# Kernel tuning notes

Hardware: AMD Instinct MI355X
Metric: run time of the kernel (lower is better)

## Reference

```python
import jax, jax.numpy as jnp
import numpy as np

B, S, D = 4, 4096, 1024
GROUP = 256
HEAD = 128
INNER = 2048


def setup_inputs() -> dict:
    key = jax.random.key(0)
    ks = jax.random.split(key, 16)
    s = 0.02
    return {
        'x': jax.random.normal(ks[0], (B, S, D), jnp.float32),
        'Wv': jax.random.normal(ks[1], (D, INNER), jnp.float32) * s,
        'bv': jnp.zeros((INNER,), jnp.float32),
        'Wg': jax.random.normal(ks[2], (D, INNER), jnp.float32) * s,
        'bg': jnp.zeros((INNER,), jnp.float32),
        'Win': jax.random.normal(ks[3], (D, HEAD), jnp.float32) * s,
        'bin_': jnp.zeros((HEAD,), jnp.float32),
        'Wout': jax.random.normal(ks[4], (INNER, D), jnp.float32) * s,
        'bout': jnp.zeros((D,), jnp.float32),
        'g_qq': 1.0 + jax.random.normal(ks[5], (HEAD,), jnp.float32) * s,
        'b_qq': jnp.zeros((HEAD,), jnp.float32),
        'g_qk': 1.0 + jax.random.normal(ks[6], (HEAD,), jnp.float32) * s,
        'b_qk': jnp.zeros((HEAD,), jnp.float32),
        'g_lq': 1.0 + jax.random.normal(ks[7], (HEAD,), jnp.float32) * s,
        'b_lq': jnp.zeros((HEAD,), jnp.float32),
        'g_lk': 1.0 + jax.random.normal(ks[8], (HEAD,), jnp.float32) * s,
        'b_lk': jnp.zeros((HEAD,), jnp.float32),
    }


def reference(x, Wv, bv, Wg, bg, Win, bin_, Wout, bout,
              g_qq, b_qq, g_qk, b_qk, g_lq, b_lq, g_lk, b_lk):
    b, s, d = x.shape
    g = s // GROUP
    xc = x.reshape(b, g, GROUP, d)                       # [B,G,C,D]
    v = jax.nn.silu(xc @ Wv + bv)                        # [B,G,C,E]
    gate = jax.nn.silu(xc @ Wg + bg)                     # [B,G,C,E]
    x_ = jax.nn.silu(xc @ Win + bin_)                    # [B,G,C,H]
    quad_q = x_ * g_qq + b_qq
    quad_k = x_ * g_qk + b_qk
    lin_q = x_ * g_lq + b_lq
    lin_k = x_ * g_lk + b_lk
    # local quadratic relu^2 attention per chunk
    scale = jnp.asarray(INNER ** 0.5, x.dtype)           # v.size(-1)**0.5
    attn = jnp.einsum('bgns,bgms->bgnm', quad_q, quad_k) / scale
    causal_mask = jnp.triu(jnp.ones((GROUP, GROUP), bool), 1)
    attn = jnp.where(causal_mask, 0.0, attn)
    attn = jnp.square(jax.nn.relu(attn))
    v_quad = jnp.einsum('bgnm,bgme->bgne', attn, v)
    # global causal linear attention: exclusive cumsum of per-chunk k^T v over chunks
    kv = jnp.einsum('bgcs,bgce->bgse', lin_k, v)         # [B,G,H,E]
    kv = jnp.cumsum(kv, axis=1) - kv                     # exclusive over chunk dim
    v_lin = jnp.einsum('bgcs,bgse->bgce', lin_q, kv)
    o = (v_quad + v_lin) * gate
    o = o @ Wout + bout
    return o.reshape(b, s, d)
```

## Files before the change

### kernel.cpp

```cpp
#include <hip/hip_runtime.h>

typedef __attribute__((ext_vector_type(8))) short short8;
typedef __attribute__((ext_vector_type(4))) float floatx4;
typedef __attribute__((ext_vector_type(4))) unsigned short ushort4v;
typedef unsigned short u16;

#define DEV __device__ __forceinline__

DEV u16 f2bf(float f) {
  unsigned int u = __float_as_uint(f);
  u += 0x7fffu + ((u >> 16) & 1u);
  return (u16)(u >> 16);
}
DEV float bf2f(u16 h) { return __uint_as_float(((unsigned int)h) << 16); }
DEV float silu_f(float x) { return x / (1.f + __expf(-x)); }
DEV floatx4 fzero() { floatx4 z = {0.f, 0.f, 0.f, 0.f}; return z; }
DEV floatx4 mfma16(short8 a, short8 b, floatx4 c) {
  return __builtin_amdgcn_mfma_f32_16x16x32_bf16(a, b, c, 0, 0, 0);
}
DEV void gll16(const void* g, void* l) {
  __builtin_amdgcn_global_load_lds((__attribute__((address_space(1))) void*)g,
                                   (__attribute__((address_space(3))) void*)l,
                                   16, 0, 0);
}

__global__ __launch_bounds__(256) void cast_x_kernel(const float* __restrict__ x,
                                                     u16* __restrict__ xb, int n4) {
  int i = blockIdx.x * 256 + threadIdx.x;
  if (i >= n4) return;
  float4 v = ((const float4*)x)[i];
  ushort4v o;
  o[0] = f2bf(v.x); o[1] = f2bf(v.y); o[2] = f2bf(v.z); o[3] = f2bf(v.w);
  *(ushort4v*)&xb[(size_t)i * 4] = o;
}

__global__ __launch_bounds__(256) void transpose_cast_kernel(const float* __restrict__ W,
                                                             u16* __restrict__ WT,
                                                             int K, int N) {
  __shared__ u16 tile[32][36];
  int n0 = blockIdx.x * 32, k0 = blockIdx.y * 32;
  int t = threadIdx.x;
  int r = t >> 3, cs = (t & 7) * 4;
  float4 v = *(const float4*)&W[(size_t)(k0 + r) * N + n0 + cs];
  tile[r][cs + 0] = f2bf(v.x);
  tile[r][cs + 1] = f2bf(v.y);
  tile[r][cs + 2] = f2bf(v.z);
  tile[r][cs + 3] = f2bf(v.w);
  __syncthreads();
  ushort4v o;
  o[0] = tile[cs + 0][r];
  o[1] = tile[cs + 1][r];
  o[2] = tile[cs + 2][r];
  o[3] = tile[cs + 3][r];
  *(ushort4v*)&WT[(size_t)(n0 + r) * K + k0 + cs] = o;
}

DEV void wave_transposed_store(u16* __restrict__ Ct, long chunk_stride,
                               const u16* trw, int chunk, int cbase, int nbase,
                               int lane) {
#pragma unroll
  for (int it = 0; it < 8; ++it) {
    int e_l = it * 8 + (lane >> 3);
    int c_off = (lane & 7) * 8;
    short8 val = *(const short8*)&trw[e_l * 72 + c_off];
    *(short8*)&Ct[(size_t)chunk * chunk_stride + (size_t)(nbase + e_l) * 256 + cbase +
                  c_off] = val;
  }
}

__global__ __launch_bounds__(256, 2) void gemm_vg(
    const u16* __restrict__ A, const u16* __restrict__ Bv, const u16* __restrict__ Bg,
    const float* __restrict__ bvb, const float* __restrict__ bgb,
    u16* __restrict__ vT, u16* __restrict__ gate) {
  constexpr int K = 1024, N = 2048;
  __shared__ union {
    struct { u16 a[128 * 64]; u16 b[2][128 * 64]; } st;
    u16 tr[4 * 64 * 72];
  } sm;
  const int t = threadIdx.x;
  const int wave = t >> 6, lane = t & 63;
  const int l15 = lane & 15, l16 = lane >> 4;
  const int ell = blockIdx.x;
  const int xcd = ell & 7, i = ell >> 3;
  const int m0 = (xcd * 16 + (i >> 4)) * 128;
  const int n0 = (i & 15) * 128;
  const int wm = (wave >> 1) * 64, wn = (wave & 1) * 64;

  floatx4 accv[4][4], accg[4][4];
#pragma unroll
  for (int a = 0; a < 4; ++a)
#pragma unroll
    for (int b = 0; b < 4; ++b) { accv[a][b] = fzero(); accg[a][b] = fzero(); }

  const u16 *pa[4], *pbv[4], *pbg[4];
#pragma unroll
  for (int j = 0; j < 4; ++j) {
    const int c = t + 256 * j;
    const int r = c >> 3, p = c & 7;
    const int g = p ^ (r & 7);
    const size_t off = (size_t)r * K + g * 8;
    pa[j] = A + (size_t)m0 * K + off;
    pbv[j] = Bv + (size_t)n0 * K + off;
    pbg[j] = Bg + (size_t)n0 * K + off;
  }

  for (int k0 = 0; k0 < K; k0 += 64) {
    __syncthreads();
#pragma unroll
    for (int j = 0; j < 4; ++j) {
      const int d = (t + 256 * j) * 8;
      gll16(pa[j] + k0, &sm.st.a[d]);
      gll16(pbv[j] + k0, &sm.st.b[0][d]);
      gll16(pbg[j] + k0, &sm.st.b[1][d]);
    }
    __syncthreads();
#pragma unroll
    for (int s = 0; s < 2; ++s) {
      short8 af[4], b0[4], b1[4];
#pragma unroll
      for (int mi = 0; mi < 4; ++mi) {
        const int wr = wm + mi * 16 + l15;
        af[mi] = *(const short8*)&sm.st.a[wr * 64 + ((s * 4 + l16) ^ (wr & 7)) * 8];
      }
#pragma unroll
      for (int ni = 0; ni < 4; ++ni) {
        const int wr = wn + ni * 16 + l15;
        const int sl = wr * 64 + ((s * 4 + l16) ^ (wr & 7)) * 8;
        b0[ni] = *(const short8*)&sm.st.b[0][sl];
        b1[ni] = *(const short8*)&sm.st.b[1][sl];
      }
#pragma unroll
      for (int mi = 0; mi < 4; ++mi)
#pragma unroll
        for (int ni = 0; ni < 4; ++ni) {
          accv[mi][ni] = mfma16(af[mi], b0[ni], accv[mi][ni]);
          accg[mi][ni] = mfma16(af[mi], b1[ni], accg[mi][ni]);
        }
    }
  }
  __syncthreads();

  u16* trw = &sm.tr[wave * 64 * 72];
#pragma unroll
  for (int mi = 0; mi < 4; ++mi)
#pragma unroll
    for (int ni = 0; ni < 4; ++ni) {
      const float bc = bvb[n0 + wn + ni * 16 + l15];
      ushort4v p;
#pragma unroll
      for (int r = 0; r < 4; ++r) p[r] = f2bf(silu_f(accv[mi][ni][r] + bc));
      *(ushort4v*)&trw[(ni * 16 + l15) * 72 + mi * 16 + l16 * 4] = p;
    }
  wave_transposed_store(vT, 2048L * 256, trw, (m0 + wm) >> 8, (m0 + wm) & 255,
                        n0 + wn, lane);
#pragma unroll
  for (int mi = 0; mi < 4; ++mi)
#pragma unroll
    for (int ni = 0; ni < 4; ++ni) {
      const float bc = bgb[n0 + wn + ni * 16 + l15];
#pragma unroll
      for (int r = 0; r < 4; ++r)
        trw[(mi * 16 + l16 * 4 + r) * 72 + ni * 16 + l15] =
            f2bf(silu_f(accg[mi][ni][r] + bc));
    }
#pragma unroll
  for (int it = 0; it < 8; ++it) {
    const int m_l = it * 8 + (lane >> 3);
    const int n_off = (lane & 7) * 8;
    *(short8*)&gate[(size_t)(m0 + wm + m_l) * N + n0 + wn + n_off] =
        *(const short8*)&trw[m_l * 72 + n_off];
  }
}

template <int MODE>
__global__ __launch_bounds__(256) void gemm_bt(
    const u16* __restrict__ A, const u16* __restrict__ Bt, int M, int N, int K,
    int nshift, const float* __restrict__ bias, u16* __restrict__ Cn,
    float* __restrict__ Cf, u16* __restrict__ Ct, long ct_stride,
    u16* __restrict__ Cn2, u16* __restrict__ Cn3,
    const float* __restrict__ gqq, const float* __restrict__ bqq,
    const float* __restrict__ gqk, const float* __restrict__ bqk,
    const float* __restrict__ glq, const float* __restrict__ blq,
    const float* __restrict__ glk, const float* __restrict__ blk) {
  __shared__ union {
    struct { u16 a[128 * 64]; u16 b[128 * 64]; } st;
    u16 tr[4 * 64 * 72];
  } sm;
  const int t = threadIdx.x;
  const int wave = t >> 6, lane = t & 63;
  const int l15 = lane & 15, l16 = lane >> 4;
  const int ell = blockIdx.x;
  const int xcd = ell & 7, i = ell >> 3;
  const int mtiles_per_xcd = M >> 10;
  const int m0 = (xcd * mtiles_per_xcd + (i >> nshift)) * 128;
  const int n0 = (i & ((1 << nshift) - 1)) * 128;
  const int wm = (wave >> 1) * 64, wn = (wave & 1) * 64;

  floatx4 acc[4][4];
#pragma unroll
  for (int i2 = 0; i2 < 4; ++i2)
#pragma unroll
    for (int j = 0; j < 4; ++j) acc[i2][j] = fzero();

  const u16* pa[4];
  const u16* pb[4];
#pragma unroll
  for (int j = 0; j < 4; ++j) {
    const int c = t + 256 * j;
    const int r = c >> 3, p = c & 7;
    const int g = p ^ (r & 7);
    pa[j] = A + (size_t)(m0 + r) * K + g * 8;
    pb[j] = Bt + (size_t)(n0 + r) * K + g * 8;
  }

  for (int k0 = 0; k0 < K; k0 += 64) {
    __syncthreads();
#pragma unroll
    for (int j = 0; j < 4; ++j) {
      gll16(pa[j] + k0, &sm.st.a[(t + 256 * j) * 8]);
      gll16(pb[j] + k0, &sm.st.b[(t + 256 * j) * 8]);
    }
    __syncthreads();
#pragma unroll
    for (int s = 0; s < 2; ++s) {
      short8 af[4], bfr[4];
#pragma unroll
      for (int mi = 0; mi < 4; ++mi) {
        const int wr = wm + mi * 16 + l15;
        af[mi] = *(const short8*)&sm.st.a[wr * 64 + ((s * 4 + l16) ^ (wr & 7)) * 8];
      }
#pragma unroll
      for (int ni = 0; ni < 4; ++ni) {
        const int wr = wn + ni * 16 + l15;
        bfr[ni] = *(const short8*)&sm.st.b[wr * 64 + ((s * 4 + l16) ^ (wr & 7)) * 8];
      }
#pragma unroll
      for (int mi = 0; mi < 4; ++mi)
#pragma unroll
        for (int ni = 0; ni < 4; ++ni)
          acc[mi][ni] = mfma16(af[mi], bfr[ni], acc[mi][ni]);
    }
  }
  __syncthreads();

  if constexpr (MODE == 3) {
#pragma unroll
    for (int mi = 0; mi < 4; ++mi)
#pragma unroll
      for (int ni = 0; ni < 4; ++ni) {
        const int col = n0 + wn + ni * 16 + l15;
        const float bc = bias[col];
        const int row = m0 + wm + mi * 16 + l16 * 4;
#pragma unroll
        for (int r = 0; r < 4; ++r)
          Cf[(size_t)(row + r) * N + col] = acc[mi][ni][r] + bc;
      }
  } else {
    u16* trw = &sm.tr[wave * 64 * 72];
#pragma unroll
    for (int mi = 0; mi < 4; ++mi)
#pragma unroll
      for (int ni = 0; ni < 4; ++ni) {
        const int col = wn + ni * 16 + l15;
        const float bc = bias[col];
        const float Gqq = gqq[col], Bqq = bqq[col];
        const float Gqk = gqk[col], Bqk = bqk[col];
        const float Glq = glq[col], Blq = blq[col];
        const float Glk = glk[col], Blk = blk[col];
        const int row = m0 + wm + mi * 16 + l16 * 4;
        ushort4v p;
#pragma unroll
        for (int r = 0; r < 4; ++r) {
          const float sv = silu_f(acc[mi][ni][r] + bc);
          const size_t ad = (size_t)(row + r) * N + col;
          Cn[ad] = f2bf(sv * Gqq + Bqq);
          Cn2[ad] = f2bf(sv * Gqk + Bqk);
          Cn3[ad] = f2bf(sv * Glq + Blq);
          p[r] = f2bf(sv * Glk + Blk);
        }
        *(ushort4v*)&trw[(ni * 16 + l15) * 72 + mi * 16 + l16 * 4] = p;
      }
    wave_transposed_store(Ct, ct_stride, trw, (m0 + wm) >> 8, (m0 + wm) & 255, wn,
                          lane);
  }
}

__global__ __launch_bounds__(256) void kv_kernel(const u16* __restrict__ vT,
                                                 const u16* __restrict__ lkT,
                                                 u16* __restrict__ kv) {
  const int chunk = blockIdx.y;
  const int et = blockIdx.x;
  const int w = threadIdx.x >> 6, lane = threadIdx.x & 63;
  const int l15 = lane & 15, l16 = lane >> 4;
  const size_t vb = (size_t)chunk * (2048 * 256) + (size_t)et * (128 * 256);
  const size_t lb = (size_t)chunk * (128 * 256);
  const int we = (w >> 1) * 64, wh = (w & 1) * 64;
  floatx4 acc[4][4];
#pragma unroll
  for (int i = 0; i < 4; ++i)
#pragma unroll
    for (int j = 0; j < 4; ++j) acc[i][j] = fzero();
  for (int kk = 0; kk < 8; ++kk) {
    short8 av[4], bv[4];
#pragma unroll
    for (int mi = 0; mi < 4; ++mi)
      av[mi] = *(const short8*)&vT[vb + (size_t)(we + mi * 16 + l15) * 256 + kk * 32 +
                                   l16 * 8];
#pragma unroll
    for (int ni = 0; ni < 4; ++ni)
      bv[ni] = *(const short8*)&lkT[lb + (size_t)(wh + ni * 16 + l15) * 256 + kk * 32 +
                                    l16 * 8];
#pragma unroll
    for (int mi = 0; mi < 4; ++mi)
#pragma unroll
      for (int ni = 0; ni < 4; ++ni) acc[mi][ni] = mfma16(av[mi], bv[ni], acc[mi][ni]);
  }
  u16* out = kv + (size_t)chunk * (2048 * 128);
#pragma unroll
  for (int mi = 0; mi < 4; ++mi)
#pragma unroll
    for (int ni = 0; ni < 4; ++ni) {
      const int h = wh + ni * 16 + l15;
      const int e = et * 128 + we + mi * 16 + l16 * 4;
#pragma unroll
      for (int r = 0; r < 4; ++r) out[(size_t)(e + r) * 128 + h] = f2bf(acc[mi][ni][r]);
    }
}

__global__ __launch_bounds__(256) void cumsum_kernel(u16* __restrict__ kv) {
  const int idx = blockIdx.x * 256 + threadIdx.x;
  const int b = blockIdx.y;
  float s = 0.f;
  for (int g = 0; g < 16; ++g) {
    const size_t a = (size_t)(b * 16 + g) * 262144 + idx;
    const float v = bf2f(kv[a]);
    kv[a] = f2bf(s);
    s += v;
  }
}

__global__ __launch_bounds__(256) void attn_kernel(
    const u16* __restrict__ qq, const u16* __restrict__ qk, const u16* __restrict__ lq,
    const u16* __restrict__ vT, const u16* __restrict__ kvT,
    u16* __restrict__ gate_op) {
  __shared__ u16 S[64][264];
  const int chunk = blockIdx.y;
  const int e0 = blockIdx.x * 256;
  const int tok0 = chunk * 256;
  const int w = threadIdx.x >> 6, lane = threadIdx.x & 63;
  const int l15 = lane & 15, l16 = lane >> 4;
  const float isc = 0.022097086912079608f;
  const size_t vbase = (size_t)chunk * (2048 * 256);
  const size_t kbase = (size_t)chunk * (2048 * 128);
  const int ew = e0 + w * 64;

  for (int ns = 0; ns < 4; ++ns) {
    const int r0 = ns * 64 + w * 16;
    short8 af[4];
#pragma unroll
    for (int kk = 0; kk < 4; ++kk)
      af[kk] = *(const short8*)&qq[(size_t)(tok0 + r0 + l15) * 128 + kk * 32 + l16 * 8];
    const int mt_cnt = (r0 >> 4) + 1;
    const int mt_all = (ns + 1) * 4;
    const int srow = w * 16 + l16 * 4;
    for (int mt = 0; mt < mt_all; ++mt) {
      if (mt < mt_cnt) {
        floatx4 a = fzero();
#pragma unroll
        for (int kk = 0; kk < 4; ++kk) {
          short8 bq =
              *(const short8*)&qk[(size_t)(tok0 + mt * 16 + l15) * 128 + kk * 32 +
                                  l16 * 8];
          a = mfma16(af[kk], bq, a);
        }
        const int mcol = mt * 16 + l15;
#pragma unroll
        for (int r = 0; r < 4; ++r) {
          const int nrow = r0 + l16 * 4 + r;
          float sv = a[r] * isc;
          sv = (mcol <= nrow) ? sv : 0.f;
          sv = fmaxf(sv, 0.f);
          S[srow + r][mcol] = f2bf(sv * sv);
        }
      } else {
#pragma unroll
        for (int r = 0; r < 4; ++r) S[srow + r][mt * 16 + l15] = (u16)0;
      }
    }
    __syncthreads();

    floatx4 acc[4][4];
#pragma unroll
    for (int i = 0; i < 4; ++i)
#pragma unroll
      for (int j = 0; j < 4; ++j) acc[i][j] = fzero();

    const int ks = (ns + 1) * 2;
    for (int kk = 0; kk < ks; ++kk) {
      short8 sa[4];
#pragma unroll
      for (int nt = 0; nt < 4; ++nt)
        sa[nt] = *(const short8*)&S[nt * 16 + l15][kk * 32 + l16 * 8];
#pragma unroll
      for (int ei = 0; ei < 4; ++ei) {
        short8 vb = *(const short8*)&vT[vbase + (size_t)(ew + ei * 16 + l15) * 256 +
                                        kk * 32 + l16 * 8];
#pragma unroll
        for (int nt = 0; nt < 4; ++nt) acc[nt][ei] = mfma16(sa[nt], vb, acc[nt][ei]);
      }
    }
#pragma unroll
    for (int kk = 0; kk < 4; ++kk) {
      short8 la[4];
#pragma unroll
      for (int nt = 0; nt < 4; ++nt)
        la[nt] = *(const short8*)&lq[(size_t)(tok0 + ns * 64 + nt * 16 + l15) * 128 +
                                     kk * 32 + l16 * 8];
#pragma unroll
      for (int ei = 0; ei < 4; ++ei) {
        short8 kb = *(const short8*)&kvT[kbase + (size_t)(ew + ei * 16 + l15) * 128 +
                                         kk * 32 + l16 * 8];
#pragma unroll
        for (int nt = 0; nt < 4; ++nt) acc[nt][ei] = mfma16(la[nt], kb, acc[nt][ei]);
      }
    }
#pragma unroll
    for (int nt = 0; nt < 4; ++nt)
#pragma unroll
      for (int ei = 0; ei < 4; ++ei) {
        const int e_g = ew + ei * 16 + l15;
        const int nb = tok0 + ns * 64 + nt * 16 + l16 * 4;
#pragma unroll
        for (int r = 0; r < 4; ++r) {
          const size_t ad = (size_t)(nb + r) * 2048 + e_g;
          const float gv = bf2f(gate_op[ad]);
          gate_op[ad] = f2bf(acc[nt][ei][r] * gv);
        }
      }
    __syncthreads();
  }
}

extern "C" void kernel_launch(void* const* d_in, const int* in_sizes, int n_in,
                              void* d_out, int out_size, void* d_ws, size_t ws_size,
                              hipStream_t stream) {
  (void)in_sizes; (void)n_in; (void)out_size; (void)ws_size;
  const float* x = (const float*)d_in[0];
  const float* Wv = (const float*)d_in[1];
  const float* bv = (const float*)d_in[2];
  const float* Wg = (const float*)d_in[3];
  const float* bg = (const float*)d_in[4];
  const float* Win = (const float*)d_in[5];
  const float* bin = (const float*)d_in[6];
  const float* Wout = (const float*)d_in[7];
  const float* bout = (const float*)d_in[8];
  const float* gqq = (const float*)d_in[9];
  const float* bqq = (const float*)d_in[10];
  const float* gqk = (const float*)d_in[11];
  const float* bqk = (const float*)d_in[12];
  const float* glq = (const float*)d_in[13];
  const float* blq = (const float*)d_in[14];
  const float* glk = (const float*)d_in[15];
  const float* blk = (const float*)d_in[16];

  char* p = (char*)d_ws;
  u16* xb = (u16*)p;   p += (size_t)16384 * 1024 * 2;
  u16* wvT = (u16*)p;  p += (size_t)2048 * 1024 * 2;
  u16* wgT = (u16*)p;  p += (size_t)2048 * 1024 * 2;
  u16* winT = (u16*)p; p += (size_t)128 * 1024 * 2;
  u16* woT = (u16*)p;  p += (size_t)1024 * 2048 * 2;
  u16* vTb = (u16*)p;  p += (size_t)64 * 2048 * 256 * 2;
  u16* gate = (u16*)p; p += (size_t)16384 * 2048 * 2;
  u16* qqb = (u16*)p;  p += (size_t)16384 * 128 * 2;
  u16* qkb = (u16*)p;  p += (size_t)16384 * 128 * 2;
  u16* lqb = (u16*)p;  p += (size_t)16384 * 128 * 2;
  u16* lkTb = (u16*)p; p += (size_t)64 * 128 * 256 * 2;
  u16* kvb = (u16*)p;  p += (size_t)64 * 2048 * 128 * 2;

  cast_x_kernel<<<16384, 256, 0, stream>>>(x, xb, 4194304);
  transpose_cast_kernel<<<dim3(64, 32), 256, 0, stream>>>(Wv, wvT, 1024, 2048);
  transpose_cast_kernel<<<dim3(64, 32), 256, 0, stream>>>(Wg, wgT, 1024, 2048);
  transpose_cast_kernel<<<dim3(4, 32), 256, 0, stream>>>(Win, winT, 1024, 128);
  transpose_cast_kernel<<<dim3(32, 64), 256, 0, stream>>>(Wout, woT, 2048, 1024);

  gemm_vg<<<2048, 256, 0, stream>>>(xb, wvT, wgT, bv, bg, vTb, gate);
  gemm_bt<2><<<128, 256, 0, stream>>>(
      xb, winT, 16384, 128, 1024, 0, bin, qqb, nullptr, lkTb, 128L * 256, qkb, lqb,
      gqq, bqq, gqk, bqk, glq, blq, glk, blk);

  kv_kernel<<<dim3(16, 64), 256, 0, stream>>>(vTb, lkTb, kvb);
  cumsum_kernel<<<dim3(1024, 4), 256, 0, stream>>>(kvb);
  attn_kernel<<<dim3(8, 64), 256, 0, stream>>>(qqb, qkb, lqb, vTb, kvb, gate);

  gemm_bt<3><<<1024, 256, 0, stream>>>(
      gate, woT, 16384, 1024, 2048, 3, bout, nullptr, (float*)d_out, nullptr, 0,
      nullptr, nullptr, nullptr, nullptr, nullptr, nullptr, nullptr, nullptr, nullptr,
      nullptr);
}
```

Baseline: 559.7 us.

## Precompute attention scores in separate kernel and widen Wout GEMM tile to 128x256

The relu² attention score matrix was previously recomputed by each of the 8 e-tile blocks per chunk. It now comes from a dedicated s_kernel that writes S once to a global buffer, and attn_kernel reads it instead of doing the QK MFMAs and syncs itself. The output projection GEMM is specialised into gemm_wout with a 128x256 tile, two accumulator sets per wave and launch_bounds(256,2), halving the block count and improving A-tile reuse. The trade-offs are extra global traffic and a launch for the S buffer, plus higher register and LDS pressure in the wider GEMM.

```diff
diff --git a/kernel.cpp b/kernel.cpp
--- a/kernel.cpp
+++ b/kernel.cpp
@@ -172,16 +172,101 @@
   }
 }
 
-template <int MODE>
-__global__ __launch_bounds__(256) void gemm_bt(
-    const u16* __restrict__ A, const u16* __restrict__ Bt, int M, int N, int K,
-    int nshift, const float* __restrict__ bias, u16* __restrict__ Cn,
-    float* __restrict__ Cf, u16* __restrict__ Ct, long ct_stride,
-    u16* __restrict__ Cn2, u16* __restrict__ Cn3,
+__global__ __launch_bounds__(256, 2) void gemm_wout(
+    const u16* __restrict__ A, const u16* __restrict__ Bt,
+    const float* __restrict__ bias, float* __restrict__ Cf) {
+  constexpr int K = 2048, N = 1024;
+  __shared__ struct { u16 a[128 * 64]; u16 b[256 * 64]; } sm;
+  const int t = threadIdx.x;
+  const int wave = t >> 6, lane = t & 63;
+  const int l15 = lane & 15, l16 = lane >> 4;
+  const int ell = blockIdx.x;
+  const int xcd = ell & 7, i = ell >> 3;
+  const int m0 = (xcd * 16 + (i >> 2)) * 128;
+  const int n0 = (i & 3) * 256;
+  const int wm = (wave >> 1) * 64, wn = (wave & 1) * 64;
+
+  floatx4 acc0[4][4], acc1[4][4];
+#pragma unroll
+  for (int a = 0; a < 4; ++a)
+#pragma unroll
+    for (int b = 0; b < 4; ++b) { acc0[a][b] = fzero(); acc1[a][b] = fzero(); }
+
+  const u16 *pa[4], *pb[8];
+#pragma unroll
+  for (int j = 0; j < 4; ++j) {
+    const int c = t + 256 * j;
+    const int r = c >> 3, p = c & 7;
+    const int g = p ^ (r & 7);
+    pa[j] = A + (size_t)(m0 + r) * K + g * 8;
+  }
+#pragma unroll
+  for (int j = 0; j < 8; ++j) {
+    const int c = t + 256 * j;
+    const int r = c >> 3, p = c & 7;
+    const int g = p ^ (r & 7);
+    pb[j] = Bt + (size_t)(n0 + r) * K + g * 8;
+  }
+
+  for (int k0 = 0; k0 < K; k0 += 64) {
+    __syncthreads();
+#pragma unroll
+    for (int j = 0; j < 4; ++j)
+      gll16(pa[j] + k0, &sm.a[(t + 256 * j) * 8]);
+#pragma unroll
+    for (int j = 0; j < 8; ++j)
+      gll16(pb[j] + k0, &sm.b[(t + 256 * j) * 8]);
+    __syncthreads();
+#pragma unroll
+    for (int s = 0; s < 2; ++s) {
+      short8 af[4], b0[4], b1[4];
+#pragma unroll
+      for (int mi = 0; mi < 4; ++mi) {
+        const int wr = wm + mi * 16 + l15;
+        af[mi] = *(const short8*)&sm.a[wr * 64 + ((s * 4 + l16) ^ (wr & 7)) * 8];
+      }
+#pragma unroll
+      for (int ni = 0; ni < 4; ++ni) {
+        const int rlo = wn + ni * 16 + l15;
+        const int rhi = rlo + 128;
+        b0[ni] = *(const short8*)&sm.b[rlo * 64 + ((s * 4 + l16) ^ (rlo & 7)) * 8];
+        b1[ni] = *(const short8*)&sm.b[rhi * 64 + ((s * 4 + l16) ^ (rhi & 7)) * 8];
+      }
+#pragma unroll
+      for (int mi = 0; mi < 4; ++mi)
+#pragma unroll
+        for (int ni = 0; ni < 4; ++ni) {
+          acc0[mi][ni] = mfma16(af[mi], b0[ni], acc0[mi][ni]);
+          acc1[mi][ni] = mfma16(af[mi], b1[ni], acc1[mi][ni]);
+        }
+    }
+  }
+
+#pragma unroll
+  for (int mi = 0; mi < 4; ++mi)
+#pragma unroll
+    for (int ni = 0; ni < 4; ++ni) {
+      const int clo = n0 + wn + ni * 16 + l15;
+      const int chi = clo + 128;
+      const float blo = bias[clo], bhi = bias[chi];
+      const int row = m0 + wm + mi * 16 + l16 * 4;
+#pragma unroll
+      for (int r = 0; r < 4; ++r) {
+        Cf[(size_t)(row + r) * N + clo] = acc0[mi][ni][r] + blo;
+        Cf[(size_t)(row + r) * N + chi] = acc1[mi][ni][r] + bhi;
+      }
+    }
+}
+
+__global__ __launch_bounds__(256) void gemm_in(
+    const u16* __restrict__ A, const u16* __restrict__ Bt,
+    const float* __restrict__ bias, u16* __restrict__ Cn, u16* __restrict__ Cn2,
+    u16* __restrict__ Cn3, u16* __restrict__ Ct,
     const float* __restrict__ gqq, const float* __restrict__ bqq,
     const float* __restrict__ gqk, const float* __restrict__ bqk,
     const float* __restrict__ glq, const float* __restrict__ blq,
     const float* __restrict__ glk, const float* __restrict__ blk) {
+  constexpr int K = 1024, N = 128;
   __shared__ union {
     struct { u16 a[128 * 64]; u16 b[128 * 64]; } st;
     u16 tr[4 * 64 * 72];
@@ -191,9 +276,7 @@
   const int l15 = lane & 15, l16 = lane >> 4;
   const int ell = blockIdx.x;
   const int xcd = ell & 7, i = ell >> 3;
-  const int mtiles_per_xcd = M >> 10;
-  const int m0 = (xcd * mtiles_per_xcd + (i >> nshift)) * 128;
-  const int n0 = (i & ((1 << nshift) - 1)) * 128;
+  const int m0 = (xcd * 16 + i) * 128;
   const int wm = (wave >> 1) * 64, wn = (wave & 1) * 64;
 
   floatx4 acc[4][4];
@@ -210,7 +293,7 @@
     const int r = c >> 3, p = c & 7;
     const int g = p ^ (r & 7);
     pa[j] = A + (size_t)(m0 + r) * K + g * 8;
-    pb[j] = Bt + (size_t)(n0 + r) * K + g * 8;
+    pb[j] = Bt + (size_t)r * K + g * 8;
   }
 
   for (int k0 = 0; k0 < K; k0 += 64) {
@@ -243,46 +326,32 @@
   }
   __syncthreads();
 
-  if constexpr (MODE == 3) {
-#pragma unroll
-    for (int mi = 0; mi < 4; ++mi)
-#pragma unroll
-      for (int ni = 0; ni < 4; ++ni) {
-        const int col = n0 + wn + ni * 16 + l15;
-        const float bc = bias[col];
-        const int row = m0 + wm + mi * 16 + l16 * 4;
-#pragma unroll
-        for (int r = 0; r < 4; ++r)
-          Cf[(size_t)(row + r) * N + col] = acc[mi][ni][r] + bc;
-      }
-  } else {
-    u16* trw = &sm.tr[wave * 64 * 72];
-#pragma unroll
-    for (int mi = 0; mi < 4; ++mi)
-#pragma unroll
-      for (int ni = 0; ni < 4; ++ni) {
-        const int col = wn + ni * 16 + l15;
-        const float bc = bias[col];
-        const float Gqq = gqq[col], Bqq = bqq[col];
-        const float Gqk = gqk[col], Bqk = bqk[col];
-        const float Glq = glq[col], Blq = blq[col];
-        const float Glk = glk[col], Blk = blk[col];
-        const int row = m0 + wm + mi * 16 + l16 * 4;
-        ushort4v p;
-#pragma unroll
-        for (int r = 0; r < 4; ++r) {
-          const float sv = silu_f(acc[mi][ni][r] + bc);
-          const size_t ad = (size_t)(row + r) * N + col;
-          Cn[ad] = f2bf(sv * Gqq + Bqq);
-          Cn2[ad] = f2bf(sv * Gqk + Bqk);
-          Cn3[ad] = f2bf(sv * Glq + Blq);
-          p[r] = f2bf(sv * Glk + Blk);
-        }
-        *(ushort4v*)&trw[(ni * 16 + l15) * 72 + mi * 16 + l16 * 4] = p;
-      }
-    wave_transposed_store(Ct, ct_stride, trw, (m0 + wm) >> 8, (m0 + wm) & 255, wn,
-                          lane);
-  }
+  u16* trw = &sm.tr[wave * 64 * 72];
+#pragma unroll
+  for (int mi = 0; mi < 4; ++mi)
+#pragma unroll
+    for (int ni = 0; ni < 4; ++ni) {
+      const int col = wn + ni * 16 + l15;
+      const float bc = bias[col];
+      const float Gqq = gqq[col], Bqq = bqq[col];
+      const float Gqk = gqk[col], Bqk = bqk[col];
+      const float Glq = glq[col], Blq = blq[col];
+      const float Glk = glk[col], Blk = blk[col];
+      const int row = m0 + wm + mi * 16 + l16 * 4;
+      ushort4v p;
+#pragma unroll
+      for (int r = 0; r < 4; ++r) {
+        const float sv = silu_f(acc[mi][ni][r] + bc);
+        const size_t ad = (size_t)(row + r) * N + col;
+        Cn[ad] = f2bf(sv * Gqq + Bqq);
+        Cn2[ad] = f2bf(sv * Gqk + Bqk);
+        Cn3[ad] = f2bf(sv * Glq + Blq);
+        p[r] = f2bf(sv * Glk + Blk);
+      }
+      *(ushort4v*)&trw[(ni * 16 + l15) * 72 + mi * 16 + l16 * 4] = p;
+    }
+  wave_transposed_store(Ct, 128L * 256, trw, (m0 + wm) >> 8, (m0 + wm) & 255, wn,
+                        lane);
 }
 
 __global__ __launch_bounds__(256) void kv_kernel(const u16* __restrict__ vT,
@@ -339,56 +408,72 @@
   }
 }
 
+__global__ __launch_bounds__(256) void s_kernel(const u16* __restrict__ qq,
+                                                const u16* __restrict__ qk,
+                                                u16* __restrict__ Sb) {
+  __shared__ u16 Sl[64][264];
+  const int ns = blockIdx.x, chunk = blockIdx.y;
+  const int tok0 = chunk * 256;
+  const int w = threadIdx.x >> 6, lane = threadIdx.x & 63;
+  const int l15 = lane & 15, l16 = lane >> 4;
+  const float isc = 0.022097086912079608f;
+
+  const int r0 = ns * 64 + w * 16;
+  short8 af[4];
+#pragma unroll
+  for (int kk = 0; kk < 4; ++kk)
+    af[kk] = *(const short8*)&qq[(size_t)(tok0 + r0 + l15) * 128 + kk * 32 + l16 * 8];
+  const int mt_cnt = (r0 >> 4) + 1;
+  const int mt_all = (ns + 1) * 4;
+  const int srow = w * 16 + l16 * 4;
+  for (int mt = 0; mt < mt_all; ++mt) {
+    if (mt < mt_cnt) {
+      floatx4 a = fzero();
+#pragma unroll
+      for (int kk = 0; kk < 4; ++kk) {
+        short8 bq = *(const short8*)&qk[(size_t)(tok0 + mt * 16 + l15) * 128 +
+                                        kk * 32 + l16 * 8];
+        a = mfma16(af[kk], bq, a);
+      }
+      const int mcol = mt * 16 + l15;
+#pragma unroll
+      for (int r = 0; r < 4; ++r) {
+        const int nrow = r0 + l16 * 4 + r;
+        float sv = a[r] * isc;
+        sv = (mcol <= nrow) ? sv : 0.f;
+        sv = fmaxf(sv, 0.f);
+        Sl[srow + r][mcol] = f2bf(sv * sv);
+      }
+    } else {
+#pragma unroll
+      for (int r = 0; r < 4; ++r) Sl[srow + r][mt * 16 + l15] = (u16)0;
+    }
+  }
+  __syncthreads();
+  u16* dst = Sb + (size_t)chunk * 65536 + (size_t)ns * 64 * 256;
+  const int cpr = (ns + 1) * 8;
+  const int total = 64 * cpr;
+  for (int idx = threadIdx.x; idx < total; idx += 256) {
+    const int row = idx / cpr, cof = (idx % cpr) * 8;
+    *(short8*)&dst[row * 256 + cof] = *(const short8*)&Sl[row][cof];
+  }
+}
+
 __global__ __launch_bounds__(256) void attn_kernel(
-    const u16* __restrict__ qq, const u16* __restrict__ qk, const u16* __restrict__ lq,
+    const u16* __restrict__ Sb, const u16* __restrict__ lq,
     const u16* __restrict__ vT, const u16* __restrict__ kvT,
     u16* __restrict__ gate_op) {
-  __shared__ u16 S[64][264];
   const int chunk = blockIdx.y;
   const int e0 = blockIdx.x * 256;
   const int tok0 = chunk * 256;
   const int w = threadIdx.x >> 6, lane = threadIdx.x & 63;
   const int l15 = lane & 15, l16 = lane >> 4;
-  const float isc = 0.022097086912079608f;
   const size_t vbase = (size_t)chunk * (2048 * 256);
   const size_t kbase = (size_t)chunk * (2048 * 128);
+  const size_t sbase = (size_t)chunk * 65536;
   const int ew = e0 + w * 64;
 
   for (int ns = 0; ns < 4; ++ns) {
-    const int r0 = ns * 64 + w * 16;
-    short8 af[4];
-#pragma unroll
-    for (int kk = 0; kk < 4; ++kk)
-      af[kk] = *(const short8*)&qq[(size_t)(tok0 + r0 + l15) * 128 + kk * 32 + l16 * 8];
-    const int mt_cnt = (r0 >> 4) + 1;
-    const int mt_all = (ns + 1) * 4;
-    const int srow = w * 16 + l16 * 4;
-    for (int mt = 0; mt < mt_all; ++mt) {
-      if (mt < mt_cnt) {
-        floatx4 a = fzero();
-#pragma unroll
-        for (int kk = 0; kk < 4; ++kk) {
-          short8 bq =
-              *(const short8*)&qk[(size_t)(tok0 + mt * 16 + l15) * 128 + kk * 32 +
-                                  l16 * 8];
-          a = mfma16(af[kk], bq, a);
-        }
-        const int mcol = mt * 16 + l15;
-#pragma unroll
-        for (int r = 0; r < 4; ++r) {
-          const int nrow = r0 + l16 * 4 + r;
-          float sv = a[r] * isc;
-          sv = (mcol <= nrow) ? sv : 0.f;
-          sv = fmaxf(sv, 0.f);
-          S[srow + r][mcol] = f2bf(sv * sv);
-        }
-      } else {
-#pragma unroll
-        for (int r = 0; r < 4; ++r) S[srow + r][mt * 16 + l15] = (u16)0;
-      }
-    }
-    __syncthreads();
-
     floatx4 acc[4][4];
 #pragma unroll
     for (int i = 0; i < 4; ++i)
@@ -400,7 +485,8 @@
       short8 sa[4];
 #pragma unroll
       for (int nt = 0; nt < 4; ++nt)
-        sa[nt] = *(const short8*)&S[nt * 16 + l15][kk * 32 + l16 * 8];
+        sa[nt] = *(const short8*)&Sb[sbase + (size_t)(ns * 64 + nt * 16 + l15) * 256 +
+                                     kk * 32 + l16 * 8];
 #pragma unroll
       for (int ei = 0; ei < 4; ++ei) {
         short8 vb = *(const short8*)&vT[vbase + (size_t)(ew + ei * 16 + l15) * 256 +
@@ -437,7 +523,6 @@
           gate_op[ad] = f2bf(acc[nt][ei][r] * gv);
         }
       }
-    __syncthreads();
   }
 }
 
@@ -476,6 +561,7 @@
   u16* lqb = (u16*)p;  p += (size_t)16384 * 128 * 2;
   u16* lkTb = (u16*)p; p += (size_t)64 * 128 * 256 * 2;
   u16* kvb = (u16*)p;  p += (size_t)64 * 2048 * 128 * 2;
+  u16* Sbuf = (u16*)p; p += (size_t)64 * 256 * 256 * 2;
 
   cast_x_kernel<<<16384, 256, 0, stream>>>(x, xb, 4194304);
   transpose_cast_kernel<<<dim3(64, 32), 256, 0, stream>>>(Wv, wvT, 1024, 2048);
@@ -484,16 +570,13 @@
   transpose_cast_kernel<<<dim3(32, 64), 256, 0, stream>>>(Wout, woT, 2048, 1024);
 
   gemm_vg<<<2048, 256, 0, stream>>>(xb, wvT, wgT, bv, bg, vTb, gate);
-  gemm_bt<2><<<128, 256, 0, stream>>>(
-      xb, winT, 16384, 128, 1024, 0, bin, qqb, nullptr, lkTb, 128L * 256, qkb, lqb,
-      gqq, bqq, gqk, bqk, glq, blq, glk, blk);
+  gemm_in<<<128, 256, 0, stream>>>(xb, winT, bin, qqb, qkb, lqb, lkTb, gqq, bqq, gqk,
+                                   bqk, glq, blq, glk, blk);
 
   kv_kernel<<<dim3(16, 64), 256, 0, stream>>>(vTb, lkTb, kvb);
   cumsum_kernel<<<dim3(1024, 4), 256, 0, stream>>>(kvb);
-  attn_kernel<<<dim3(8, 64), 256, 0, stream>>>(qqb, qkb, lqb, vTb, kvb, gate);
-
-  gemm_bt<3><<<1024, 256, 0, stream>>>(
-      gate, woT, 16384, 1024, 2048, 3, bout, nullptr, (float*)d_out, nullptr, 0,
-      nullptr, nullptr, nullptr, nullptr, nullptr, nullptr, nullptr, nullptr, nullptr,
-      nullptr);
-}
+  s_kernel<<<dim3(4, 64), 256, 0, stream>>>(qqb, qkb, Sbuf);
+  attn_kernel<<<dim3(8, 64), 256, 0, stream>>>(Sbuf, lqb, vTb, kvb, gate);
+
+  gemm_wout<<<512, 256, 0, stream>>>(gate, woT, bout, (float*)d_out);
+}
```

Result: no change. 569.3 us (+1.7%).
